# Performance work log

Hardware: AMD Instinct MI355X
Metric: run time of the kernel (lower is better)

## Reference

```python
import jax, jax.numpy as jnp
import numpy as np

DT = 0.01
NT = 2000
B = 16384


def setup_inputs() -> dict:
    key = jax.random.key(0)
    k1, k2 = jax.random.split(key)
    x0 = jax.random.normal(k1, (B, 3), dtype=jnp.float32)
    p = jax.random.uniform(k2, (3,), dtype=jnp.float32) * 10.0  # matches torch.rand(3)*10
    return {"x0": x0, "p": p}


def _yp(X, p):
    # Lorenz RHS, X: [B, 3]
    x, y, z = X[:, 0], X[:, 1], X[:, 2]
    return jnp.stack([p[0] * (y - x), x * (p[1] - z) - y, x * y - p[2] * z], axis=1)


def reference(x0, p):
    dt = jnp.float32(DT)

    def step(Xi, _):
        k1 = _yp(Xi, p)
        k2 = _yp(Xi + dt / 2 * k1, p)
        k3 = _yp(Xi + dt / 2 * k2, p)
        k4 = _yp(Xi + dt * k3, p)
        Xn = Xi + dt / 6 * (k1 + 2 * k2 + 2 * k3 + k4)
        return Xn, Xn

    _, traj = jax.lax.scan(step, x0, None, length=NT)  # [NT, B, 3]
    X = jnp.concatenate([x0[None], traj], axis=0)      # [NT+1, B, 3]
    return jnp.transpose(X, (1, 2, 0))                  # [B, 3, NT+1]
```

## Files before the change

### kernel.cpp

```cpp
#include <hip/hip_runtime.h>


#define NT     2000
#define TT     64
#define NFULL  31
#define TAIL   16
#define TROWS  2001
#define ROWS   64
#define LROWS  65

#define FMA(a,b,c) __builtin_fmaf((a),(b),(c))

__global__ __launch_bounds__(192) void lorenz_rk4(
    const float* __restrict__ x0,
    const float* __restrict__ p,
    float* __restrict__ out)
{
#pragma clang fp contract(off)
    __shared__ float buf[2][3][TT][LROWS];

    const int tid  = threadIdx.x;
    const int lane = tid & 63;
    const int b0   = blockIdx.x * ROWS;

    if (tid < 64) {
        const float p0  = p[0], p1 = p[1], p2n = -p[2];
        const float h1 = 0.01f;
        const float h2 = 0.01f / 2.0f;
        const float h6 = 0.01f / 6.0f;
        const int b = b0 + lane;
        float x = x0[3*b + 0], y = x0[3*b + 1], z = x0[3*b + 2];

        {
            size_t g = (size_t)b * (3 * TROWS);
            out[g] = x; out[g + TROWS] = y; out[g + 2*TROWS] = z;
        }

#define STEP() do {                                                          \
        float k1x = p0 * (y - x);                                            \
        float k1y = FMA(x, p1 - z, -y);                                      \
        float k1z = FMA(p2n, z, x * y);                                      \
        float ax = FMA(h2,k1x,x), ay = FMA(h2,k1y,y), az = FMA(h2,k1z,z);    \
        float k2x = p0 * (ay - ax);                                          \
        float k2y = FMA(ax, p1 - az, -ay);                                   \
        float k2z = FMA(p2n, az, ax * ay);                                   \
        float bx = FMA(h2,k2x,x), by = FMA(h2,k2y,y), bz = FMA(h2,k2z,z);    \
        float k3x = p0 * (by - bx);                                          \
        float k3y = FMA(bx, p1 - bz, -by);                                   \
        float k3z = FMA(p2n, bz, bx * by);                                   \
        float cx = FMA(h1,k3x,x), cy = FMA(h1,k3y,y), cz = FMA(h1,k3z,z);    \
        float k4x = p0 * (cy - cx);                                          \
        float k4y = FMA(cx, p1 - cz, -cy);                                   \
        float k4z = FMA(p2n, cz, cx * cy);                                   \
        float sx = FMA(2.0f,k2x,k1x); sx = FMA(2.0f,k3x,sx); sx += k4x;      \
        float sy = FMA(2.0f,k2y,k1y); sy = FMA(2.0f,k3y,sy); sy += k4y;      \
        float sz = FMA(2.0f,k2z,k1z); sz = FMA(2.0f,k3z,sz); sz += k4z;      \
        x = FMA(h6,sx,x); y = FMA(h6,sy,y); z = FMA(h6,sz,z);                \
    } while (0)

        for (int k = 0; k < NFULL; ++k) {
            float* bb = &buf[k & 1][0][0][0];
#pragma unroll 16
            for (int tl = 0; tl < TT; ++tl) {
                STEP();
                bb[              tl*LROWS + lane] = x;
                bb[  TT*LROWS  + tl*LROWS + lane] = y;
                bb[2*TT*LROWS  + tl*LROWS + lane] = z;
            }
            __syncthreads();
        }
#pragma unroll 16
        for (int tl = 0; tl < TAIL; ++tl) {
            STEP();
            buf[1][0][tl][lane] = x;
            buf[1][1][tl][lane] = y;
            buf[1][2][tl][lane] = z;
        }
        __syncthreads();
#undef STEP
    } else {
        const int w     = (tid >> 6) - 1;
        const int rbase = w * 32;
        const int t     = lane;

        for (int k = 0; k < NFULL; ++k) {
            __syncthreads();
            const float* bb = &buf[k & 1][0][0][0];
            size_t g = (size_t)(b0 + rbase) * (3 * TROWS) + 1 + (size_t)k * TT + t;
#pragma unroll 4
            for (int r = rbase; r < rbase + 32; ++r) {
                out[g]             = bb[              t*LROWS + r];
                out[g +     TROWS] = bb[  TT*LROWS  + t*LROWS + r];
                out[g + 2 * TROWS] = bb[2*TT*LROWS  + t*LROWS + r];
                g += (size_t)(3 * TROWS);
            }
        }
        __syncthreads();
        {
            const int tloc = lane & 15;
            int rloc = rbase + (lane >> 4);
            size_t g = (size_t)(b0 + rloc) * (3 * TROWS) + 1 + (size_t)NFULL * TT + tloc;
#pragma unroll 4
            for (int i = 0; i < 8; ++i) {
                out[g]             = buf[1][0][tloc][rloc];
                out[g +     TROWS] = buf[1][1][tloc][rloc];
                out[g + 2 * TROWS] = buf[1][2][tloc][rloc];
                rloc += 4;
                g    += (size_t)4 * (3 * TROWS);
            }
        }
    }
}

extern "C" void kernel_launch(void* const* d_in, const int* in_sizes, int n_in,
                              void* d_out, int out_size, void* d_ws, size_t ws_size,
                              hipStream_t stream)
{
    const float* x0  = (const float*)d_in[0];
    const float* p   = (const float*)d_in[1];
    float*       out = (float*)d_out;

    const int B = in_sizes[0] / 3;
    const int nblocks = B / ROWS;

    lorenz_rk4<<<nblocks, 192, 0, stream>>>(x0, p, out);
}
```

Before: 172.9 us.

## Split time integration into checkpoint pass plus two parallel half-trajectory passes

Adds a coarse kernel that integrates each trajectory for the first 1000 steps without storing anything and writes a checkpoint state to workspace. A second kernel then launches twice as many blocks, so each trajectory's two halves are integrated and written out in parallel, one from x0 and one from the checkpoint. The goal is more parallelism: the original 256 blocks cannot fill the GPU. The cost is recomputing the first half of the trajectory and paying for an extra kernel launch. The transpose tile is also reduced to 32 timesteps with a remapped store loop.

```diff
diff --git a/kernel.cpp b/kernel.cpp
--- a/kernel.cpp
+++ b/kernel.cpp
@@ -1,40 +1,15 @@
 #include <hip/hip_runtime.h>
 
 
-#define NT     2000
-#define TT     64
-#define NFULL  31
-#define TAIL   16
 #define TROWS  2001
 #define ROWS   64
 #define LROWS  65
+#define TT     32
+#define HALF   1000
+#define NFULL  31
+#define TAIL   8
 
 #define FMA(a,b,c) __builtin_fmaf((a),(b),(c))
-
-__global__ __launch_bounds__(192) void lorenz_rk4(
-    const float* __restrict__ x0,
-    const float* __restrict__ p,
-    float* __restrict__ out)
-{
-#pragma clang fp contract(off)
-    __shared__ float buf[2][3][TT][LROWS];
-
-    const int tid  = threadIdx.x;
-    const int lane = tid & 63;
-    const int b0   = blockIdx.x * ROWS;
-
-    if (tid < 64) {
-        const float p0  = p[0], p1 = p[1], p2n = -p[2];
-        const float h1 = 0.01f;
-        const float h2 = 0.01f / 2.0f;
-        const float h6 = 0.01f / 6.0f;
-        const int b = b0 + lane;
-        float x = x0[3*b + 0], y = x0[3*b + 1], z = x0[3*b + 2];
-
-        {
-            size_t g = (size_t)b * (3 * TROWS);
-            out[g] = x; out[g + TROWS] = y; out[g + 2*TROWS] = z;
-        }
 
 #define STEP() do {                                                          \
         float k1x = p0 * (y - x);                                            \
@@ -58,9 +33,54 @@
         x = FMA(h6,sx,x); y = FMA(h6,sy,y); z = FMA(h6,sz,z);                \
     } while (0)
 
+__global__ __launch_bounds__(64) void lorenz_coarse(
+    const float* __restrict__ x0,
+    const float* __restrict__ p,
+    float* __restrict__ ckpt)
+{
+#pragma clang fp contract(off)
+    const int lane = threadIdx.x;
+    const int b = blockIdx.x * 64 + lane;
+    const float p0 = p[0], p1 = p[1], p2n = -p[2];
+    const float h1 = 0.01f, h2 = 0.01f / 2.0f, h6 = 0.01f / 6.0f;
+    float x = x0[3*b + 0], y = x0[3*b + 1], z = x0[3*b + 2];
+
+#pragma unroll 8
+    for (int t = 0; t < HALF; ++t) STEP();
+
+    ckpt[3*b + 0] = x; ckpt[3*b + 1] = y; ckpt[3*b + 2] = z;
+}
+
+__global__ __launch_bounds__(192) void lorenz_fine(
+    const float* __restrict__ x0,
+    const float* __restrict__ p,
+    const float* __restrict__ ckpt,
+    float* __restrict__ out)
+{
+#pragma clang fp contract(off)
+    __shared__ float buf[2][3][TT][LROWS];
+
+    const int tid  = threadIdx.x;
+    const int lane = tid & 63;
+    const int half = blockIdx.x >> 8;
+    const int b0   = (blockIdx.x & 255) * ROWS;
+    const size_t obase = (size_t)half * HALF;
+
+    if (tid < 64) {
+        const float p0 = p[0], p1 = p[1], p2n = -p[2];
+        const float h1 = 0.01f, h2 = 0.01f / 2.0f, h6 = 0.01f / 6.0f;
+        const int b = b0 + lane;
+        const float* src = half ? ckpt : x0;
+        float x = src[3*b + 0], y = src[3*b + 1], z = src[3*b + 2];
+
+        if (!half) {
+            size_t g = (size_t)b * (3 * TROWS);
+            out[g] = x; out[g + TROWS] = y; out[g + 2*TROWS] = z;
+        }
+
         for (int k = 0; k < NFULL; ++k) {
             float* bb = &buf[k & 1][0][0][0];
-#pragma unroll 16
+#pragma unroll 8
             for (int tl = 0; tl < TT; ++tl) {
                 STEP();
                 bb[              tl*LROWS + lane] = x;
@@ -69,7 +89,7 @@
             }
             __syncthreads();
         }
-#pragma unroll 16
+#pragma unroll
         for (int tl = 0; tl < TAIL; ++tl) {
             STEP();
             buf[1][0][tl][lane] = x;
@@ -77,36 +97,39 @@
             buf[1][2][tl][lane] = z;
         }
         __syncthreads();
-#undef STEP
     } else {
         const int w     = (tid >> 6) - 1;
         const int rbase = w * 32;
-        const int t     = lane;
+        const int tloc  = lane & 31;
+        const int rofs  = lane >> 5;
 
         for (int k = 0; k < NFULL; ++k) {
             __syncthreads();
             const float* bb = &buf[k & 1][0][0][0];
-            size_t g = (size_t)(b0 + rbase) * (3 * TROWS) + 1 + (size_t)k * TT + t;
+            int r = rbase + rofs;
+            size_t g = (size_t)(b0 + r) * (3 * TROWS) + obase + 1 + (size_t)k * TT + tloc;
 #pragma unroll 4
-            for (int r = rbase; r < rbase + 32; ++r) {
-                out[g]             = bb[              t*LROWS + r];
-                out[g +     TROWS] = bb[  TT*LROWS  + t*LROWS + r];
-                out[g + 2 * TROWS] = bb[2*TT*LROWS  + t*LROWS + r];
-                g += (size_t)(3 * TROWS);
+            for (int i = 0; i < 16; ++i) {
+                out[g]             = bb[              tloc*LROWS + r];
+                out[g +     TROWS] = bb[  TT*LROWS  + tloc*LROWS + r];
+                out[g + 2 * TROWS] = bb[2*TT*LROWS  + tloc*LROWS + r];
+                r += 2;
+                g += (size_t)2 * (3 * TROWS);
             }
         }
         __syncthreads();
         {
-            const int tloc = lane & 15;
-            int rloc = rbase + (lane >> 4);
-            size_t g = (size_t)(b0 + rloc) * (3 * TROWS) + 1 + (size_t)NFULL * TT + tloc;
-#pragma unroll 4
-            for (int i = 0; i < 8; ++i) {
-                out[g]             = buf[1][0][tloc][rloc];
-                out[g +     TROWS] = buf[1][1][tloc][rloc];
-                out[g + 2 * TROWS] = buf[1][2][tloc][rloc];
-                rloc += 4;
-                g    += (size_t)4 * (3 * TROWS);
+            const float* bb = &buf[1][0][0][0];
+            const int tt = lane & 7;
+            int r = rbase + (lane >> 3);
+            size_t g = (size_t)(b0 + r) * (3 * TROWS) + obase + 1 + (size_t)NFULL * TT + tt;
+#pragma unroll
+            for (int i = 0; i < 4; ++i) {
+                out[g]             = bb[              tt*LROWS + r];
+                out[g +     TROWS] = bb[  TT*LROWS  + tt*LROWS + r];
+                out[g + 2 * TROWS] = bb[2*TT*LROWS  + tt*LROWS + r];
+                r += 8;
+                g += (size_t)8 * (3 * TROWS);
             }
         }
     }
@@ -119,9 +142,11 @@
     const float* x0  = (const float*)d_in[0];
     const float* p   = (const float*)d_in[1];
     float*       out = (float*)d_out;
+    float*       ckpt = (float*)d_ws;
 
     const int B = in_sizes[0] / 3;
-    const int nblocks = B / ROWS;
+    const int nb = B / ROWS;
 
-    lorenz_rk4<<<nblocks, 192, 0, stream>>>(x0, p, out);
+    lorenz_coarse<<<nb,     64, 0, stream>>>(x0, p, ckpt);
+    lorenz_fine  <<<2 * nb, 192, 0, stream>>>(x0, p, ckpt, out);
 }
```

Result: slower. 263.4 us, median of 5 (+52.3%).
